# Optimization experiments

Hardware: AMD Instinct MI355X
Metric: run time of the kernel (lower is better)

Reference implementation:

```python
import jax, jax.numpy as jnp
import numpy as np
from jax import lax

B, N, C = 8, 3136, 512
NUM_HEADS = 8
HEAD_DIM = C // NUM_HEADS
KS = 5  # depthwise conv kernel size


def setup_inputs() -> dict:
    key = jax.random.key(0)
    ks = jax.random.split(key, 8)
    s = 0.02
    return {
        "x": jax.random.normal(ks[0], (B, N, C), dtype=jnp.float32),
        "H": 56,
        "W": 56,
        "Wq": jax.random.normal(ks[1], (C, C), dtype=jnp.float32) * s,
        "Wkv": jax.random.normal(ks[2], (C, 2 * C), dtype=jnp.float32) * s,
        "pos_enc": jnp.zeros((1, N, C), dtype=jnp.float32),
        "dwc_w": jax.random.normal(ks[3], (HEAD_DIM, 1, KS, KS), dtype=jnp.float32) * s,
        "dwc_b": jnp.zeros((HEAD_DIM,), dtype=jnp.float32),
        "Wproj": jax.random.normal(ks[4], (C, C), dtype=jnp.float32) * s,
        "bproj": jnp.zeros((C,), dtype=jnp.float32),
    }


def _split_heads(t):
    # (B, N, C) -> (B*h, N, head_dim), matching 'b n (h c) -> (b h) n c'
    b, n, c = t.shape
    return t.reshape(b, n, NUM_HEADS, HEAD_DIM).transpose(0, 2, 1, 3).reshape(b * NUM_HEADS, n, HEAD_DIM)


def reference(x, H, W, Wq, Wkv, pos_enc, dwc_w, dwc_b, Wproj, bproj):
    b, n, c = x.shape
    # projections (qkv_bias=False)
    q = jnp.maximum(x @ Wq, 0.0)                       # ReLU kernel feature map
    kv = x @ Wkv
    k = jnp.maximum(kv[..., :c] + pos_enc, 0.0)
    v = kv[..., c:]

    q = _split_heads(q)  # (bh, n, d)
    k = _split_heads(k)
    v = _split_heads(v)

    # normalizer z_i = 1 / (q_i . sum_j k_j + eps)
    z = 1.0 / (jnp.einsum('bic,bc->bi', q, k.sum(axis=1)) + 1e-6)
    # kv-first ordering (i*j*(c+d) > c*d*(i+j) for these shapes)
    kvmat = jnp.einsum('bjc,bjd->bcd', k, v)           # (bh, d, d)
    out = jnp.einsum('bic,bcd->bid', q, kvmat) * z[..., None]

    # depthwise conv residual on v: 'b (w h) c -> b c w h'
    num = int(round(n ** 0.5))
    fmap = v.reshape(-1, num, num, HEAD_DIM).transpose(0, 3, 1, 2)  # (bh, d, num, num)
    fmap = lax.conv_general_dilated(
        fmap, dwc_w, window_strides=(1, 1), padding='SAME',
        feature_group_count=HEAD_DIM,
        dimension_numbers=('NCHW', 'OIHW', 'NCHW'))
    fmap = fmap + dwc_b[None, :, None, None]
    fmap = fmap.transpose(0, 2, 3, 1).reshape(-1, n, HEAD_DIM)
    out = out + fmap

    # merge heads: '(b h) n c -> b n (h c)'
    out = out.reshape(b, NUM_HEADS, n, HEAD_DIM).transpose(0, 2, 1, 3).reshape(b, n, c)
    return out @ Wproj + bproj
```

## Files before the change

### kernel.cpp

```cpp
#include <hip/hip_runtime.h>
#include <stdint.h>

#define B_    8
#define N_    3136
#define C_    512
#define MTOT  25088

typedef __attribute__((ext_vector_type(8))) short bf16x8;
typedef __attribute__((ext_vector_type(4))) float f32x4;

__device__ __forceinline__ float bf2f(short s){
  union { float f; uint32_t u; } cv; cv.u = ((uint32_t)(uint16_t)s) << 16; return cv.f;
}
__device__ __forceinline__ short f2bf(float f){
  union { float f; uint32_t u; } cv; cv.f = f;
  uint32_t r = cv.u + 0x7FFFu + ((cv.u >> 16) & 1u);
  return (short)(r >> 16);
}

typedef const __attribute__((address_space(1))) void* gas1_t;
typedef __attribute__((address_space(3))) void* las3_t;
__device__ __forceinline__ void gld16(const void* g, void* l){
  __builtin_amdgcn_global_load_lds((gas1_t)g, (las3_t)l, 16, 0, 0);
}

#define BARR  __builtin_amdgcn_s_barrier()
#define SCHB  __builtin_amdgcn_sched_barrier(0)
#define VMC0  asm volatile("s_waitcnt vmcnt(0)" ::: "memory")
#define VMC2  asm volatile("s_waitcnt vmcnt(2)" ::: "memory")
#define VMC3  asm volatile("s_waitcnt vmcnt(3)" ::: "memory")
#define LGKM0 asm volatile("s_waitcnt lgkmcnt(0)" ::: "memory")

__global__ __launch_bounds__(256) void cvt_x(const float* __restrict__ x,
                                             short* __restrict__ xb, int n8){
  int i = blockIdx.x * 256 + threadIdx.x;
  if (i >= n8) return;
  const float4* p = (const float4*)x;
  float4 a = p[i*2], b = p[i*2+1];
  short o[8] = { f2bf(a.x), f2bf(a.y), f2bf(a.z), f2bf(a.w),
                 f2bf(b.x), f2bf(b.y), f2bf(b.z), f2bf(b.w) };
  *(bf16x8*)(xb + i*8) = *(bf16x8*)o;
}

__global__ __launch_bounds__(256) void tconv(const float* __restrict__ src,
                                             short* __restrict__ dst, int J){
  __shared__ float tile[32][33];
  int jb = blockIdx.x * 32, kb = blockIdx.y * 32;
  int tx = threadIdx.x & 31, ty = threadIdx.x >> 5;
#pragma unroll
  for (int r = 0; r < 32; r += 8)
    tile[ty + r][tx] = src[(size_t)(kb + ty + r) * J + jb + tx];
  __syncthreads();
#pragma unroll
  for (int r = 0; r < 32; r += 8)
    dst[(size_t)(jb + ty + r) * 512 + kb + tx] = f2bf(tile[tx][ty + r]);
}

__global__ __launch_bounds__(256) void conv_wT(const float* __restrict__ w,
                                               float* __restrict__ wt){
  int i = blockIdx.x * 256 + threadIdx.x;
  if (i < 1600) { int c = i / 25, tap = i - c * 25; wt[tap * 64 + c] = w[i]; }
}

template<int MODE, int NCT>
__global__ __launch_bounds__(512, 4)
void gemm_bf16(const short* __restrict__ A, const short* __restrict__ Bt,
               short* __restrict__ oQ, short* __restrict__ oK, short* __restrict__ oV,
               const float* __restrict__ posenc,
               float* __restrict__ oF, const float* __restrict__ bias)
{
  constexpr int BN    = MODE ? 128 : 256;
  constexpr int NJ    = MODE ? 2 : 4;
  constexpr int WNW   = MODE ? 32 : 64;
  constexpr int BUFSZ = MODE ? 16384 : 24576;
  constexpr int BOFF  = 8192;
  extern __shared__ __align__(16) char lds[];
  const int tid = threadIdx.x;
  const int wave = tid >> 6, lane = tid & 63;
  const int fr = lane & 15;

  constexpr int nwg = 196 * NCT;
  constexpr int q8 = nwg / 8, r8 = nwg % 8;
  const int orig = blockIdx.x;
  const int xcd = orig & 7, lid = orig >> 3;
  const int swz = (xcd < r8 ? xcd * (q8 + 1) : r8 * (q8 + 1) + (xcd - r8) * q8) + lid;
  const int rt = (swz / NCT) * 128;
  const int ct = (swz % NCT) * BN;

  const int wm = (wave >> 2) * 64;
  const int wn = (wave & 3) * WNW;

  const int srow = lane >> 2;
  const int csrc = ((lane & 3) ^ ((lane >> 3) & 3)) << 3;
  const short* srcA = A  + (size_t)(rt + wave * 16 + srow) * 512 + csrc;
  const short* srcB = Bt + (size_t)(ct + wave * (MODE ? 16 : 32) + srow) * 512 + csrc;
  char* dA = lds + wave * 1024;
  char* dB = lds + BOFF + wave * (MODE ? 1024 : 2048);

  auto stage = [&](int t) {
    const int b = (t % 3) * BUFSZ;
    const short* a0 = srcA + t * 32;
    gld16(a0, dA + b);
    const short* b0 = srcB + t * 32;
    gld16(b0, dB + b);
    if (MODE == 0) gld16(b0 + 8192, dB + b + 1024);
  };

  const int cR   = (((lane >> 4) ^ ((fr >> 1) & 3)) << 4);
  const int offA = (wm + fr) * 64 + cR;
  const int offB = BOFF + (wn + fr) * 64 + cR;

  f32x4 zv = {0.f, 0.f, 0.f, 0.f};
  f32x4 acc[4][NJ];
#pragma unroll
  for (int i = 0; i < 4; i++)
#pragma unroll
    for (int j = 0; j < NJ; j++) acc[i][j] = zv;

  stage(0); stage(1);

#pragma unroll
  for (int t = 0; t < 16; ++t) {
    if (t < 15) { if (MODE == 0) { VMC3; } else { VMC2; } }
    else       { VMC0; }
    BARR; SCHB;
    if (t + 2 < 16) stage(t + 2);
    const char* sb = lds + (t % 3) * BUFSZ;
    bf16x8 af[4], bfr[NJ];
#pragma unroll
    for (int i = 0; i < 4; i++) af[i] = *(const bf16x8*)(sb + offA + i * 1024);
#pragma unroll
    for (int j = 0; j < NJ; j++) bfr[j] = *(const bf16x8*)(sb + offB + j * 1024);
    LGKM0; SCHB;
    __builtin_amdgcn_s_setprio(1);
#pragma unroll
    for (int i = 0; i < 4; i++)
#pragma unroll
      for (int j = 0; j < NJ; j++)
        acc[i][j] = __builtin_amdgcn_mfma_f32_16x16x32_bf16(af[i], bfr[j], acc[i][j], 0, 0, 0);
    __builtin_amdgcn_s_setprio(0);
  }

  BARR; SCHB;

  const int rb = (lane >> 4) << 2;
  if (MODE == 0) {
    short* ov = (short*)lds;
    const int sel = ct >> 9;
    const int cb  = ct - sel * 512;
    short* outp = sel == 0 ? oQ : (sel == 1 ? oK : oV);
#pragma unroll
    for (int i = 0; i < 4; i++)
#pragma unroll
      for (int j = 0; j < 4; j++)
#pragma unroll
        for (int r = 0; r < 4; r++)
          ov[(wm + i * 16 + rb + r) * 264 + wn + j * 16 + fr] = f2bf(acc[i][j][r]);
    __syncthreads();
#pragma unroll
    for (int p = 0; p < 8; ++p) {
      int id = tid + 512 * p;
      int row = id >> 5, cc = (id & 31) * 8;
      bf16x8 vv = *(const bf16x8*)&ov[row * 264 + cc];
      int grow = rt + row;
      short o[8];
      if (sel == 0) {
#pragma unroll
        for (int e = 0; e < 8; e++) o[e] = f2bf(fmaxf(bf2f(vv[e]), 0.f));
      } else if (sel == 1) {
        int nr = grow % N_;
        const float* pp = posenc + (size_t)nr * 512 + cb + cc;
        f32x4 p0 = *(const f32x4*)pp;
        f32x4 p1 = *(const f32x4*)(pp + 4);
#pragma unroll
        for (int e = 0; e < 4; e++) {
          o[e]     = f2bf(fmaxf(bf2f(vv[e]) + p0[e], 0.f));
          o[e + 4] = f2bf(fmaxf(bf2f(vv[e + 4]) + p1[e], 0.f));
        }
      } else {
#pragma unroll
        for (int e = 0; e < 8; e++) o[e] = vv[e];
      }
      *(bf16x8*)(outp + (size_t)grow * 512 + cb + cc) = *(bf16x8*)o;
    }
  } else {
    float* ovf = (float*)lds;
#pragma unroll
    for (int i = 0; i < 4; i++)
#pragma unroll
      for (int j = 0; j < 2; j++)
#pragma unroll
        for (int r = 0; r < 4; r++)
          ovf[(wm + i * 16 + rb + r) * 132 + wn + j * 16 + fr] = acc[i][j][r];
    __syncthreads();
#pragma unroll
    for (int p = 0; p < 4; ++p) {
      int id = tid + 512 * p;
      int row = id >> 4, cc = (id & 15) * 8;
      f32x4 v0 = *(const f32x4*)&ovf[row * 132 + cc];
      f32x4 v1 = *(const f32x4*)&ovf[row * 132 + cc + 4];
      v0 += *(const f32x4*)&bias[ct + cc];
      v1 += *(const f32x4*)&bias[ct + cc + 4];
      float* op = oF + (size_t)(rt + row) * 512 + ct + cc;
      *(f32x4*)op       = v0;
      *(f32x4*)(op + 4) = v1;
    }
  }
}

__global__ __launch_bounds__(256)
void kvmat_mfma(const short* __restrict__ kb, const short* __restrict__ vb,
                float* __restrict__ pKV, float* __restrict__ pKS)
{
  __shared__ __align__(16) short lkT[64 * 72];
  __shared__ __align__(16) short lvT[64 * 72];
  const int chunk = blockIdx.x, bh = blockIdx.y;
  const int b = bh >> 3, h = bh & 7;
  const int t = threadIdx.x;
  const int wave = t >> 6, lane = t & 63;
  const int fr = lane & 15, kg = lane >> 4;

  f32x4 zv = {0.f, 0.f, 0.f, 0.f};
  f32x4 acc[4];
#pragma unroll
  for (int j = 0; j < 4; j++) acc[j] = zv;
  f32x4 accks = zv;

  bf16x8 ones;
#pragma unroll
  for (int e = 0; e < 8; e++) ones[e] = (short)0x3F80;

  const int rr = t >> 3, c8 = t & 7;
  for (int tile = 0; tile < 7; ++tile) {
    const int r0 = chunk * 448 + tile * 64;
    __syncthreads();
#pragma unroll
    for (int half = 0; half < 2; ++half) {
      int r = rr + half * 32;
      size_t g = (size_t)(b * N_ + r0 + r) * 512 + h * 64 + c8 * 8;
      bf16x8 kk = *(const bf16x8*)(kb + g);
      bf16x8 vv = *(const bf16x8*)(vb + g);
#pragma unroll
      for (int e = 0; e < 8; e++) {
        lkT[(c8 * 8 + e) * 72 + r] = kk[e];
        lvT[(c8 * 8 + e) * 72 + r] = vv[e];
      }
    }
    __syncthreads();
#pragma unroll
    for (int ks = 0; ks < 2; ++ks) {
      const int ko = ks * 32 + kg * 8;
      bf16x8 af = *(const bf16x8*)&lkT[(wave * 16 + fr) * 72 + ko];
      bf16x8 bm[4];
#pragma unroll
      for (int j = 0; j < 4; j++)
        bm[j] = *(const bf16x8*)&lvT[(j * 16 + fr) * 72 + ko];
#pragma unroll
      for (int j = 0; j < 4; j++)
        acc[j] = __builtin_amdgcn_mfma_f32_16x16x32_bf16(af, bm[j], acc[j], 0, 0, 0);
      accks = __builtin_amdgcn_mfma_f32_16x16x32_bf16(af, ones, accks, 0, 0, 0);
    }
  }

  const int pbase = (bh * 7 + chunk) * 4096;
  const int crow = wave * 16 + kg * 4;
#pragma unroll
  for (int j = 0; j < 4; j++)
#pragma unroll
    for (int r_ = 0; r_ < 4; r_++)
      pKV[pbase + (crow + r_) * 64 + j * 16 + fr] = acc[j][r_];
  if (fr == 0) {
#pragma unroll
    for (int r_ = 0; r_ < 4; r_++)
      pKS[(bh * 7 + chunk) * 64 + crow + r_] = accks[r_];
  }
}

__global__ __launch_bounds__(256)
void kv_reduce(const float* __restrict__ pKV, const float* __restrict__ pKS,
               short* __restrict__ kvT, float* __restrict__ ksum)
{
  int bh = blockIdx.x, t = threadIdx.x;
#pragma unroll
  for (int i = 0; i < 16; i++) {
    int idx = t + i * 256;
    float s = 0.f;
#pragma unroll
    for (int c = 0; c < 7; c++) s += pKV[(bh * 7 + c) * 4096 + idx];
    int cc = idx >> 6, d = idx & 63;
    kvT[bh * 4096 + d * 64 + cc] = f2bf(s);
  }
  if (t < 64) {
    float s = 0.f;
#pragma unroll
    for (int c = 0; c < 7; c++) s += pKS[(bh * 7 + c) * 64 + t];
    ksum[bh * 64 + t] = s;
  }
}

__global__ __launch_bounds__(256)
void conv_dw(const short* __restrict__ vb, const float* __restrict__ wT,
             const float* __restrict__ bias, short* __restrict__ pre)
{
  __shared__ __align__(16) short lsv[5 * 56 * 64];
  __shared__ __align__(16) float lwT[25 * 64];
  const int y = blockIdx.x, bh = blockIdx.y;
  const int b = bh >> 3, h = bh & 7;
  const int t = threadIdx.x;
  for (int i = t; i < 1600; i += 256) lwT[i] = wT[i];
  for (int i = t; i < 2240; i += 256) {
    int row = i / 448, rem = i - row * 448;
    int xx = rem >> 3, c8i = rem & 7;
    int gy = y + row - 2;
    bf16x8 val = {0, 0, 0, 0, 0, 0, 0, 0};
    if ((unsigned)gy < 56u)
      val = *(const bf16x8*)(vb + (size_t)(b * N_ + gy * 56 + xx) * 512 + h * 64 + c8i * 8);
    *(bf16x8*)(lsv + i * 8) = val;
  }
  __syncthreads();

  const int c8 = t & 7;
  const int x0 = t >> 3;
  float acc0[8], acc1[8];
  {
    f32x4 b0 = *(const f32x4*)&bias[c8 * 8];
    f32x4 b1 = *(const f32x4*)&bias[c8 * 8 + 4];
#pragma unroll
    for (int e = 0; e < 4; e++) { acc0[e] = b0[e]; acc0[e+4] = b1[e];
                                  acc1[e] = b0[e]; acc1[e+4] = b1[e]; }
  }
#pragma unroll
  for (int dy = 0; dy < 5; ++dy) {
#pragma unroll
    for (int dx = 0; dx < 5; ++dx) {
      float w8[8];
      {
        const float* wp = &lwT[(dy * 5 + dx) * 64 + c8 * 8];
        *(f32x4*)&w8[0] = *(const f32x4*)wp;
        *(f32x4*)&w8[4] = *(const f32x4*)(wp + 4);
      }
      const int base = dy * 56 * 64 + c8 * 8;
      int xxa = x0 + dx - 2;
      if ((unsigned)xxa < 56u) {
        bf16x8 v = *(const bf16x8*)(lsv + base + xxa * 64);
#pragma unroll
        for (int e = 0; e < 8; e++) acc0[e] += bf2f(v[e]) * w8[e];
      }
      int xxb = xxa + 32;
      if (xxb < 56) {
        bf16x8 v = *(const bf16x8*)(lsv + base + xxb * 64);
#pragma unroll
        for (int e = 0; e < 8; e++) acc1[e] += bf2f(v[e]) * w8[e];
      }
    }
  }
  size_t gbase = (size_t)(b * N_ + y * 56 + x0) * 512 + h * 64 + c8 * 8;
  short o[8];
#pragma unroll
  for (int e = 0; e < 8; e++) o[e] = f2bf(acc0[e]);
  *(bf16x8*)(pre + gbase) = *(bf16x8*)o;
  if (x0 + 32 < 56) {
#pragma unroll
    for (int e = 0; e < 8; e++) o[e] = f2bf(acc1[e]);
    *(bf16x8*)(pre + gbase + (size_t)32 * 512) = *(bf16x8*)o;
  }
}

__global__ __launch_bounds__(64)
void attn_mfma(const short* __restrict__ qb, const short* __restrict__ kvT,
               const float* __restrict__ ksum, short* __restrict__ pre)
{
  __shared__ __align__(16) float ov[64 * 68];
  __shared__ float lks[64];
  const int pt = blockIdx.x, bh = blockIdx.y;
  const int b = bh >> 3, h = bh & 7;
  const int l = threadIdx.x;
  const int fr = l & 15, kg = l >> 4;
  const int n0 = pt * 64;

  lks[l] = ksum[bh * 64 + l];

  const short* qbase = qb + (size_t)(b * N_ + n0) * 512 + h * 64;
  const short* kvb   = kvT + bh * 4096;
  bf16x8 af[4][2], bm[4][2];
#pragma unroll
  for (int i = 0; i < 4; i++)
#pragma unroll
    for (int s = 0; s < 2; s++) {
      af[i][s] = *(const bf16x8*)(qbase + (size_t)(fr + i * 16) * 512 + s * 32 + kg * 8);
      bm[i][s] = *(const bf16x8*)(kvb + (fr + i * 16) * 64 + s * 32 + kg * 8);
    }

  f32x4 zv4 = {0.f, 0.f, 0.f, 0.f};
  f32x4 acc[4][4];
#pragma unroll
  for (int i = 0; i < 4; i++)
#pragma unroll
    for (int j = 0; j < 4; j++) acc[i][j] = zv4;
#pragma unroll
  for (int s = 0; s < 2; s++)
#pragma unroll
    for (int i = 0; i < 4; i++)
#pragma unroll
      for (int j = 0; j < 4; j++)
        acc[i][j] = __builtin_amdgcn_mfma_f32_16x16x32_bf16(af[i][s], bm[j][s], acc[i][j], 0, 0, 0);

  const short* qrow = qb + (size_t)(b * N_ + n0 + l) * 512 + h * 64;
  float zd = 0.f;
#pragma unroll
  for (int g = 0; g < 8; g++) {
    bf16x8 qv = *(const bf16x8*)(qrow + g * 8);
#pragma unroll
    for (int e = 0; e < 8; e++) zd += bf2f(qv[e]) * lks[g * 8 + e];
  }
  const float z = 1.f / (zd + 1e-6f);

  const int rb = kg << 2;
#pragma unroll
  for (int i = 0; i < 4; i++)
#pragma unroll
    for (int j = 0; j < 4; j++)
#pragma unroll
      for (int r = 0; r < 4; r++)
        ov[(i * 16 + rb + r) * 68 + j * 16 + fr] = acc[i][j][r];
  __syncthreads();

  size_t gb = (size_t)(b * N_ + n0 + l) * 512 + h * 64;
  const float* ovr = &ov[l * 68];
#pragma unroll
  for (int g = 0; g < 8; g++) {
    bf16x8 pv = *(const bf16x8*)(pre + gb + g * 8);
    f32x4 a0 = *(const f32x4*)(ovr + g * 8);
    f32x4 a1 = *(const f32x4*)(ovr + g * 8 + 4);
    short o[8];
#pragma unroll
    for (int e = 0; e < 4; e++) {
      o[e]     = f2bf(a0[e] * z + bf2f(pv[e]));
      o[e + 4] = f2bf(a1[e] * z + bf2f(pv[e + 4]));
    }
    *(bf16x8*)(pre + gb + g * 8) = *(bf16x8*)o;
  }
}

extern "C" void kernel_launch(void* const* d_in, const int* in_sizes, int n_in,
                              void* d_out, int out_size, void* d_ws, size_t ws_size,
                              hipStream_t stream)
{
  const float* x     = (const float*)d_in[0];
  const float* Wq    = (const float*)d_in[3];
  const float* Wkv   = (const float*)d_in[4];
  const float* pos   = (const float*)d_in[5];
  const float* dwcw  = (const float*)d_in[6];
  const float* dwcb  = (const float*)d_in[7];
  const float* Wproj = (const float*)d_in[8];
  const float* bproj = (const float*)d_in[9];
  float* out = (float*)d_out;

  char* ws = (char*)d_ws;
  size_t off = 0;
  auto alloc = [&](size_t bytes) -> void* {
    void* p = ws + off;
    off = (off + bytes + 255) & ~(size_t)255;
    return p;
  };
  short* xb     = (short*)alloc((size_t)MTOT * 512 * 2);
  short* wqkvT  = (short*)alloc((size_t)1536 * 512 * 2);
  short* wprojT = (short*)alloc((size_t)512 * 512 * 2);
  float* wTc    = (float*)alloc((size_t)25 * 64 * 4);
  short* qb     = (short*)alloc((size_t)MTOT * 512 * 2);
  short* kbuf   = (short*)alloc((size_t)MTOT * 512 * 2);
  short* vbuf   = (short*)alloc((size_t)MTOT * 512 * 2);
  float* pKV    = (float*)alloc((size_t)64 * 7 * 4096 * 4);
  float* pKS    = (float*)alloc((size_t)64 * 7 * 64 * 4);
  short* kvT    = (short*)alloc((size_t)64 * 4096 * 2);
  float* ksumB  = (float*)alloc((size_t)64 * 64 * 4);
  short* pre    = (short*)alloc((size_t)MTOT * 512 * 2);
  if (ws_size < off) return;

  {
    auto k0 = gemm_bf16<0, 6>;
    auto k1 = gemm_bf16<1, 4>;
    hipFuncSetAttribute(reinterpret_cast<const void*>(k0),
                        hipFuncAttributeMaxDynamicSharedMemorySize, 73728);
    hipFuncSetAttribute(reinterpret_cast<const void*>(k1),
                        hipFuncAttributeMaxDynamicSharedMemorySize, 67584);
  }

  cvt_x<<<dim3((MTOT * 512 / 8 + 255) / 256), dim3(256), 0, stream>>>(x, xb, MTOT * 512 / 8);
  conv_wT<<<dim3(7), dim3(256), 0, stream>>>(dwcw, wTc);
  tconv<<<dim3(16, 16), dim3(256), 0, stream>>>(Wq,    wqkvT,              512);
  tconv<<<dim3(32, 16), dim3(256), 0, stream>>>(Wkv,   wqkvT + 512 * 512, 1024);
  tconv<<<dim3(16, 16), dim3(256), 0, stream>>>(Wproj, wprojT,             512);
  gemm_bf16<0, 6><<<dim3(1176), dim3(512), 73728, stream>>>(xb, wqkvT, qb, kbuf, vbuf, pos,
                                                            nullptr, nullptr);
  kvmat_mfma<<<dim3(7, 64), dim3(256), 0, stream>>>(kbuf, vbuf, pKV, pKS);
  kv_reduce<<<dim3(64), dim3(256), 0, stream>>>(pKV, pKS, kvT, ksumB);
  conv_dw<<<dim3(56, 64), dim3(256), 0, stream>>>(vbuf, wTc, dwcb, pre);
  attn_mfma<<<dim3(49, 64), dim3(64), 0, stream>>>(qb, kvT, ksumB, pre);
  gemm_bf16<1, 4><<<dim3(784), dim3(512), 67584, stream>>>(pre, wprojT, nullptr, nullptr, nullptr,
                                                           nullptr, out, bproj);
}
```

Measured before the change: 204.0 us.

## Merge prep kernels into one launch and halve output-stage LDS in proj GEMM

Folds the x-to-bf16 conversion, the three weight transposes and the conv-weight reorder into a single prep kernel that dispatches on block index, replacing five launches with one. The projection GEMM epilogue now stages its fp32 tile through LDS in two 64-row halves, which lowers the dynamic shared memory request from 67584 to 49152 bytes and may let more blocks fit per CU. The cost is an extra barrier and a serialized second pass in the epilogue.

```diff
diff --git a/kernel.cpp b/kernel.cpp
--- a/kernel.cpp
+++ b/kernel.cpp
@@ -31,22 +31,37 @@
 #define VMC3  asm volatile("s_waitcnt vmcnt(3)" ::: "memory")
 #define LGKM0 asm volatile("s_waitcnt lgkmcnt(0)" ::: "memory")
 
-__global__ __launch_bounds__(256) void cvt_x(const float* __restrict__ x,
-                                             short* __restrict__ xb, int n8){
-  int i = blockIdx.x * 256 + threadIdx.x;
-  if (i >= n8) return;
-  const float4* p = (const float4*)x;
-  float4 a = p[i*2], b = p[i*2+1];
-  short o[8] = { f2bf(a.x), f2bf(a.y), f2bf(a.z), f2bf(a.w),
-                 f2bf(b.x), f2bf(b.y), f2bf(b.z), f2bf(b.w) };
-  *(bf16x8*)(xb + i*8) = *(bf16x8*)o;
-}
-
-__global__ __launch_bounds__(256) void tconv(const float* __restrict__ src,
-                                             short* __restrict__ dst, int J){
+__global__ __launch_bounds__(256)
+void prep(const float* __restrict__ x, short* __restrict__ xb,
+          const float* __restrict__ Wq, const float* __restrict__ Wkv,
+          const float* __restrict__ Wproj, short* __restrict__ wqkvT,
+          short* __restrict__ wprojT,
+          const float* __restrict__ dwcw, float* __restrict__ wTc)
+{
   __shared__ float tile[32][33];
-  int jb = blockIdx.x * 32, kb = blockIdx.y * 32;
-  int tx = threadIdx.x & 31, ty = threadIdx.x >> 5;
+  int bid = blockIdx.x;
+  const int t = threadIdx.x;
+  if (bid < 6272) {
+    int i = bid * 256 + t;
+    const float4* p = (const float4*)x;
+    float4 a = p[i*2], b = p[i*2+1];
+    short o[8] = { f2bf(a.x), f2bf(a.y), f2bf(a.z), f2bf(a.w),
+                   f2bf(b.x), f2bf(b.y), f2bf(b.z), f2bf(b.w) };
+    *(bf16x8*)(xb + i*8) = *(bf16x8*)o;
+    return;
+  }
+  bid -= 6272;
+  if (bid >= 1024) {
+    int i = (bid - 1024) * 256 + t;
+    if (i < 1600) { int c = i / 25, tap = i - c * 25; wTc[tap * 64 + c] = dwcw[i]; }
+    return;
+  }
+  const float* src; short* dst; int J, gx;
+  if (bid < 256)      {             src = Wq;    dst = wqkvT;             J = 512;  gx = 16; }
+  else if (bid < 768) { bid -= 256; src = Wkv;   dst = wqkvT + 512 * 512; J = 1024; gx = 32; }
+  else                { bid -= 768; src = Wproj; dst = wprojT;            J = 512;  gx = 16; }
+  int jb = (bid % gx) * 32, kb = (bid / gx) * 32;
+  int tx = t & 31, ty = t >> 5;
 #pragma unroll
   for (int r = 0; r < 32; r += 8)
     tile[ty + r][tx] = src[(size_t)(kb + ty + r) * J + jb + tx];
@@ -54,12 +69,6 @@
 #pragma unroll
   for (int r = 0; r < 32; r += 8)
     dst[(size_t)(jb + ty + r) * 512 + kb + tx] = f2bf(tile[tx][ty + r]);
-}
-
-__global__ __launch_bounds__(256) void conv_wT(const float* __restrict__ w,
-                                               float* __restrict__ wt){
-  int i = blockIdx.x * 256 + threadIdx.x;
-  if (i < 1600) { int c = i / 25, tap = i - c * 25; wt[tap * 64 + c] = w[i]; }
 }
 
 template<int MODE, int NCT>
@@ -186,24 +195,30 @@
   } else {
     float* ovf = (float*)lds;
 #pragma unroll
-    for (int i = 0; i < 4; i++)
-#pragma unroll
-      for (int j = 0; j < 2; j++)
-#pragma unroll
-        for (int r = 0; r < 4; r++)
-          ovf[(wm + i * 16 + rb + r) * 132 + wn + j * 16 + fr] = acc[i][j][r];
-    __syncthreads();
-#pragma unroll
-    for (int p = 0; p < 4; ++p) {
-      int id = tid + 512 * p;
-      int row = id >> 4, cc = (id & 15) * 8;
-      f32x4 v0 = *(const f32x4*)&ovf[row * 132 + cc];
-      f32x4 v1 = *(const f32x4*)&ovf[row * 132 + cc + 4];
-      v0 += *(const f32x4*)&bias[ct + cc];
-      v1 += *(const f32x4*)&bias[ct + cc + 4];
-      float* op = oF + (size_t)(rt + row) * 512 + ct + cc;
-      *(f32x4*)op       = v0;
-      *(f32x4*)(op + 4) = v1;
+    for (int hf = 0; hf < 2; ++hf) {
+      if (hf) __syncthreads();
+      if ((wave >> 2) == hf) {
+#pragma unroll
+        for (int i = 0; i < 4; i++)
+#pragma unroll
+          for (int j = 0; j < 2; j++)
+#pragma unroll
+            for (int r = 0; r < 4; r++)
+              ovf[(i * 16 + rb + r) * 132 + wn + j * 16 + fr] = acc[i][j][r];
+      }
+      __syncthreads();
+#pragma unroll
+      for (int p = 0; p < 2; ++p) {
+        int id = tid + 512 * p;
+        int row = id >> 4, cc = (id & 15) * 8;
+        f32x4 v0 = *(const f32x4*)&ovf[row * 132 + cc];
+        f32x4 v1 = *(const f32x4*)&ovf[row * 132 + cc + 4];
+        v0 += *(const f32x4*)&bias[ct + cc];
+        v1 += *(const f32x4*)&bias[ct + cc + 4];
+        float* op = oF + (size_t)(rt + hf * 64 + row) * 512 + ct + cc;
+        *(f32x4*)op       = v0;
+        *(f32x4*)(op + 4) = v1;
+      }
     }
   }
 }
@@ -483,20 +498,17 @@
     hipFuncSetAttribute(reinterpret_cast<const void*>(k0),
                         hipFuncAttributeMaxDynamicSharedMemorySize, 73728);
     hipFuncSetAttribute(reinterpret_cast<const void*>(k1),
-                        hipFuncAttributeMaxDynamicSharedMemorySize, 67584);
-  }
-
-  cvt_x<<<dim3((MTOT * 512 / 8 + 255) / 256), dim3(256), 0, stream>>>(x, xb, MTOT * 512 / 8);
-  conv_wT<<<dim3(7), dim3(256), 0, stream>>>(dwcw, wTc);
-  tconv<<<dim3(16, 16), dim3(256), 0, stream>>>(Wq,    wqkvT,              512);
-  tconv<<<dim3(32, 16), dim3(256), 0, stream>>>(Wkv,   wqkvT + 512 * 512, 1024);
-  tconv<<<dim3(16, 16), dim3(256), 0, stream>>>(Wproj, wprojT,             512);
+                        hipFuncAttributeMaxDynamicSharedMemorySize, 49152);
+  }
+
+  prep<<<dim3(7303), dim3(256), 0, stream>>>(x, xb, Wq, Wkv, Wproj,
+                                             wqkvT, wprojT, dwcw, wTc);
   gemm_bf16<0, 6><<<dim3(1176), dim3(512), 73728, stream>>>(xb, wqkvT, qb, kbuf, vbuf, pos,
                                                             nullptr, nullptr);
   kvmat_mfma<<<dim3(7, 64), dim3(256), 0, stream>>>(kbuf, vbuf, pKV, pKS);
   kv_reduce<<<dim3(64), dim3(256), 0, stream>>>(pKV, pKS, kvT, ksumB);
   conv_dw<<<dim3(56, 64), dim3(256), 0, stream>>>(vbuf, wTc, dwcb, pre);
   attn_mfma<<<dim3(49, 64), dim3(64), 0, stream>>>(qb, kvT, ksumB, pre);
-  gemm_bf16<1, 4><<<dim3(784), dim3(512), 67584, stream>>>(pre, wprojT, nullptr, nullptr, nullptr,
+  gemm_bf16<1, 4><<<dim3(784), dim3(512), 49152, stream>>>(pre, wprojT, nullptr, nullptr, nullptr,
                                                            nullptr, out, bproj);
 }
```

After: 193.9 us. -5.0%, faster.
